# Kernel optimization log

Measured on AMD Instinct MI355X. Metric: run time of the kernel, lower is better.

Reference implementation:

```python
import jax, jax.numpy as jnp
import numpy as np

B, S, H2 = 32, 8192, 256  # batch, max_enc_steps, 2*hidden_dim
INIT_STD = 1e-4           # trunc_norm_init_std


def setup_inputs() -> dict:
    key = jax.random.key(0)
    k1, k2, k3 = jax.random.split(key, 3)
    h_d_t = jax.random.normal(k1, (B, H2), dtype=jnp.float32)
    h_enc = jax.random.normal(k2, (B, S, H2), dtype=jnp.float32)
    enc_padding_mask = jnp.ones((B, S), dtype=jnp.float32)
    sum_exp_att = jnp.ones((B, S), dtype=jnp.float32)
    # Bilinear weight (attn_dim=1 squeezed): (2H, 2H), trunc-normal init
    W = jax.random.normal(k3, (H2, H2), dtype=jnp.float32) * INIT_STD
    return {"h_d_t": h_d_t, "h_enc": h_enc, "enc_padding_mask": enc_padding_mask,
            "sum_exp_att": sum_exp_att, "W": W}


def reference(h_d_t, h_enc, enc_padding_mask, sum_exp_att, W):
    # Batched bilinear scores: score[b,s] = h_d_t[b] @ W @ h_enc[b,s]
    # replaces the per-timestep nn.Bilinear loop with one fused contraction.
    scores = jnp.einsum('bd,de,bse->bs', h_d_t, W, h_enc)  # (B, S)
    exp_att = jnp.exp(scores)
    # intra-temporal normalization by accumulated past exp attention
    att = exp_att / sum_exp_att
    new_sum_exp_att = sum_exp_att + exp_att
    # mask pads and renormalize
    alphat_e = att * enc_padding_mask
    alphat_e = alphat_e / jnp.sum(alphat_e, axis=1, keepdims=True)
    # context vector: weighted sum over encoder states
    ct_e = jnp.einsum('bs,bsd->bd', alphat_e, h_enc)  # (B, 2H)
    return ct_e, alphat_e, new_sum_exp_att
```

## Files before the change

### kernel.cpp

```cpp
#include <hip/hip_runtime.h>

#define B_ 32
#define S_ 8192
#define H_ 256

__global__ __launch_bounds__(256) void gemv_hdtW(
    const float* __restrict__ hdt,
    const float* __restrict__ W,
    float* __restrict__ v)
{
    const int b  = blockIdx.x;
    const int ec = blockIdx.y;
    const int d  = threadIdx.x;

    __shared__ float lh[32];
    if (d < 32) lh[d] = hdt[b * H_ + ec * 32 + d];
    __syncthreads();

    float acc = 0.f;
    const float* Wp = W + (size_t)(ec * 32) * H_ + d;
#pragma unroll
    for (int e = 0; e < 32; ++e) acc = fmaf(lh[e], Wp[(size_t)e * H_], acc);

    atomicAdd(&v[b * H_ + d], acc);
}

__global__ __launch_bounds__(256) void attn_main(
    const float* __restrict__ v,
    const float* __restrict__ h_enc,
    const float* __restrict__ sum_exp,
    const float* __restrict__ mask,
    float* __restrict__ out_alphat,
    float* __restrict__ out_newsum,
    float* __restrict__ denom,
    float* __restrict__ ct_un)
{
    constexpr int WAVES = 4;
    constexpr int SPB   = S_ / 32;

    const int b    = blockIdx.y;
    const int tid  = threadIdx.x;
    const int lane = tid & 63;
    const int wave = tid >> 6;
    const int s0   = blockIdx.x * SPB;

    const float4 vf = reinterpret_cast<const float4*>(v + b * H_)[lane];

    const float* __restrict__ hb  = h_enc  + (size_t)b * S_ * H_;
    const float* __restrict__ seb = sum_exp + (size_t)b * S_;
    const float* __restrict__ mkb = mask    + (size_t)b * S_;
    float* __restrict__ oab = out_alphat + (size_t)b * S_;
    float* __restrict__ onb = out_newsum + (size_t)b * S_;

    float4 ct  = {0.f, 0.f, 0.f, 0.f};
    float  den = 0.f;

    for (int i = 0; i < SPB / WAVES; ++i) {
        const int s = s0 + wave + WAVES * i;
        const float4 hf = reinterpret_cast<const float4*>(hb + (size_t)s * H_)[lane];

        float dot = fmaf(vf.x, hf.x, fmaf(vf.y, hf.y, fmaf(vf.z, hf.z, vf.w * hf.w)));
#pragma unroll
        for (int off = 32; off; off >>= 1) dot += __shfl_xor(dot, off, 64);

        const float se  = seb[s];
        const float e   = __expf(dot);
        const float att = e / se * mkb[s];

        if (lane == 0) {
            oab[s] = att;
            onb[s] = se + e;
        }
        den += att;
        ct.x = fmaf(att, hf.x, ct.x);
        ct.y = fmaf(att, hf.y, ct.y);
        ct.z = fmaf(att, hf.z, ct.z);
        ct.w = fmaf(att, hf.w, ct.w);
    }

    __shared__ __align__(16) float lct[WAVES * H_];
    __shared__ float lden[WAVES];
    reinterpret_cast<float4*>(lct + wave * H_)[lane] = ct;
    if (lane == 0) lden[wave] = den;
    __syncthreads();

    const float s4 = lct[tid] + lct[H_ + tid] + lct[2 * H_ + tid] + lct[3 * H_ + tid];
    atomicAdd(&ct_un[b * H_ + tid], s4);
    if (tid == 0) atomicAdd(&denom[b], lden[0] + lden[1] + lden[2] + lden[3]);
}

__global__ __launch_bounds__(256) void finalize(
    const float* __restrict__ denom,
    const float* __restrict__ ct_un,
    float* __restrict__ out_ct,
    float* __restrict__ out_alphat)
{
    const int idx = blockIdx.x * blockDim.x + threadIdx.x;
    if (idx < B_ * H_) {
        out_ct[idx] = ct_un[idx] / denom[idx >> 8];
    } else {
        const int p = idx - B_ * H_;
        if (p < B_ * S_) {
            out_alphat[p] = out_alphat[p] / denom[p >> 13];
        }
    }
}

extern "C" void kernel_launch(void* const* d_in, const int* in_sizes, int n_in,
                              void* d_out, int out_size, void* d_ws, size_t ws_size,
                              hipStream_t stream) {
    const float* h_d_t   = (const float*)d_in[0];
    const float* h_enc   = (const float*)d_in[1];
    const float* mask    = (const float*)d_in[2];
    const float* sum_exp = (const float*)d_in[3];
    const float* W       = (const float*)d_in[4];

    float* out        = (float*)d_out;
    float* out_ct     = out;
    float* out_alphat = out + B_ * H_;
    float* out_newsum = out + B_ * H_ + B_ * S_;

    float* ws    = (float*)d_ws;
    float* denom = ws;
    float* ct_un = ws + B_;
    float* v     = ws + B_ + B_ * H_;
    hipMemsetAsync(d_ws, 0, (size_t)(B_ + 2 * B_ * H_) * sizeof(float), stream);

    gemv_hdtW<<<dim3(B_, 8), 256, 0, stream>>>(h_d_t, W, v);
    attn_main<<<dim3(32, B_), 256, 0, stream>>>(v, h_enc, sum_exp, mask,
                                                out_alphat, out_newsum, denom, ct_un);
    const int fin_n = B_ * H_ + B_ * S_;
    finalize<<<(fin_n + 255) / 256, 256, 0, stream>>>(denom, ct_un, out_ct, out_alphat);
}
```

Baseline: 375.5 us.

## Split attention rows across 16-lane groups with smaller blocks and staged outputs

Restructures attn_main so that each 16-lane subgroup handles one encoder row, loading four float4s per lane. The dot-product reduction drops to four shuffles instead of six. Blocks now cover 128 rows rather than 256, which doubles the grid, and launch bounds request higher occupancy. The sum_exp and mask values are preloaded into shared memory, and alphat/newsum are staged there so they can be written back coalesced instead of by single lanes. The costs are more registers per thread, a 16-way shared-memory reduction of ct, and twice as many atomics.

```diff
diff --git a/kernel.cpp b/kernel.cpp
--- a/kernel.cpp
+++ b/kernel.cpp
@@ -3,6 +3,8 @@
 #define B_ 32
 #define S_ 8192
 #define H_ 256
+
+#define SPB 128
 
 __global__ __launch_bounds__(256) void gemv_hdtW(
     const float* __restrict__ hdt,
@@ -25,7 +27,7 @@
     atomicAdd(&v[b * H_ + d], acc);
 }
 
-__global__ __launch_bounds__(256) void attn_main(
+__global__ __launch_bounds__(256, 5) void attn_main(
     const float* __restrict__ v,
     const float* __restrict__ h_enc,
     const float* __restrict__ sum_exp,
@@ -35,58 +37,103 @@
     float* __restrict__ denom,
     float* __restrict__ ct_un)
 {
-    constexpr int WAVES = 4;
-    constexpr int SPB   = S_ / 32;
-
     const int b    = blockIdx.y;
     const int tid  = threadIdx.x;
     const int lane = tid & 63;
     const int wave = tid >> 6;
+    const int sub  = lane & 15;
+    const int grp  = lane >> 4;
+    const int pid  = wave * 4 + grp;
     const int s0   = blockIdx.x * SPB;
 
-    const float4 vf = reinterpret_cast<const float4*>(v + b * H_)[lane];
+    __shared__ float lmult[SPB];
+    __shared__ float lse[SPB];
+    __shared__ float lalpha[SPB];
+    __shared__ float lnew[SPB];
+    __shared__ __align__(16) float lct[16][H_];
+    __shared__ float lden[16];
 
-    const float* __restrict__ hb  = h_enc  + (size_t)b * S_ * H_;
-    const float* __restrict__ seb = sum_exp + (size_t)b * S_;
-    const float* __restrict__ mkb = mask    + (size_t)b * S_;
-    float* __restrict__ oab = out_alphat + (size_t)b * S_;
-    float* __restrict__ onb = out_newsum + (size_t)b * S_;
+    if (tid < SPB) {
+        const float se = sum_exp[(size_t)b * S_ + s0 + tid];
+        const float mk = mask[(size_t)b * S_ + s0 + tid];
+        lse[tid]   = se;
+        lmult[tid] = mk / se;
+    }
+    __syncthreads();
 
-    float4 ct  = {0.f, 0.f, 0.f, 0.f};
+    const float4* v4 = reinterpret_cast<const float4*>(v + b * H_);
+    const float4 vf0 = v4[0 * 16 + sub];
+    const float4 vf1 = v4[1 * 16 + sub];
+    const float4 vf2 = v4[2 * 16 + sub];
+    const float4 vf3 = v4[3 * 16 + sub];
+
+    const float* __restrict__ hb = h_enc + (size_t)b * S_ * H_;
+
+    float4 ct0 = {0.f,0.f,0.f,0.f}, ct1 = {0.f,0.f,0.f,0.f};
+    float4 ct2 = {0.f,0.f,0.f,0.f}, ct3 = {0.f,0.f,0.f,0.f};
     float  den = 0.f;
 
-    for (int i = 0; i < SPB / WAVES; ++i) {
-        const int s = s0 + wave + WAVES * i;
-        const float4 hf = reinterpret_cast<const float4*>(hb + (size_t)s * H_)[lane];
+#pragma unroll 2
+    for (int i = 0; i < SPB / 16; ++i) {
+        const int lr = i * 16 + wave * 4 + grp;
+        const float4* h4 = reinterpret_cast<const float4*>(hb + (size_t)(s0 + lr) * H_);
+        const float4 h0 = h4[0 * 16 + sub];
+        const float4 h1 = h4[1 * 16 + sub];
+        const float4 h2 = h4[2 * 16 + sub];
+        const float4 h3 = h4[3 * 16 + sub];
 
-        float dot = fmaf(vf.x, hf.x, fmaf(vf.y, hf.y, fmaf(vf.z, hf.z, vf.w * hf.w)));
-#pragma unroll
-        for (int off = 32; off; off >>= 1) dot += __shfl_xor(dot, off, 64);
+        float dot;
+        dot = fmaf(vf0.x, h0.x, fmaf(vf0.y, h0.y, fmaf(vf0.z, h0.z, vf0.w * h0.w)));
+        dot = fmaf(vf1.x, h1.x, fmaf(vf1.y, h1.y, fmaf(vf1.z, h1.z, fmaf(vf1.w, h1.w, dot))));
+        dot = fmaf(vf2.x, h2.x, fmaf(vf2.y, h2.y, fmaf(vf2.z, h2.z, fmaf(vf2.w, h2.w, dot))));
+        dot = fmaf(vf3.x, h3.x, fmaf(vf3.y, h3.y, fmaf(vf3.z, h3.z, fmaf(vf3.w, h3.w, dot))));
 
-        const float se  = seb[s];
+        dot += __shfl_xor(dot, 1, 16);
+        dot += __shfl_xor(dot, 2, 16);
+        dot += __shfl_xor(dot, 4, 16);
+        dot += __shfl_xor(dot, 8, 16);
+
         const float e   = __expf(dot);
-        const float att = e / se * mkb[s];
-
-        if (lane == 0) {
-            oab[s] = att;
-            onb[s] = se + e;
+        const float att = e * lmult[lr];
+        if (sub == 0) {
+            lalpha[lr] = att;
+            lnew[lr]   = lse[lr] + e;
         }
         den += att;
-        ct.x = fmaf(att, hf.x, ct.x);
-        ct.y = fmaf(att, hf.y, ct.y);
-        ct.z = fmaf(att, hf.z, ct.z);
-        ct.w = fmaf(att, hf.w, ct.w);
+        ct0.x = fmaf(att, h0.x, ct0.x); ct0.y = fmaf(att, h0.y, ct0.y);
+        ct0.z = fmaf(att, h0.z, ct0.z); ct0.w = fmaf(att, h0.w, ct0.w);
+        ct1.x = fmaf(att, h1.x, ct1.x); ct1.y = fmaf(att, h1.y, ct1.y);
+        ct1.z = fmaf(att, h1.z, ct1.z); ct1.w = fmaf(att, h1.w, ct1.w);
+        ct2.x = fmaf(att, h2.x, ct2.x); ct2.y = fmaf(att, h2.y, ct2.y);
+        ct2.z = fmaf(att, h2.z, ct2.z); ct2.w = fmaf(att, h2.w, ct2.w);
+        ct3.x = fmaf(att, h3.x, ct3.x); ct3.y = fmaf(att, h3.y, ct3.y);
+        ct3.z = fmaf(att, h3.z, ct3.z); ct3.w = fmaf(att, h3.w, ct3.w);
     }
 
-    __shared__ __align__(16) float lct[WAVES * H_];
-    __shared__ float lden[WAVES];
-    reinterpret_cast<float4*>(lct + wave * H_)[lane] = ct;
-    if (lane == 0) lden[wave] = den;
+    float4* dst = reinterpret_cast<float4*>(&lct[pid][0]);
+    dst[0 * 16 + sub] = ct0;
+    dst[1 * 16 + sub] = ct1;
+    dst[2 * 16 + sub] = ct2;
+    dst[3 * 16 + sub] = ct3;
+    if (sub == 0) lden[pid] = den;
     __syncthreads();
 
-    const float s4 = lct[tid] + lct[H_ + tid] + lct[2 * H_ + tid] + lct[3 * H_ + tid];
-    atomicAdd(&ct_un[b * H_ + tid], s4);
-    if (tid == 0) atomicAdd(&denom[b], lden[0] + lden[1] + lden[2] + lden[3]);
+    float tot = 0.f;
+#pragma unroll
+    for (int p = 0; p < 16; ++p) tot += lct[p][tid];
+    atomicAdd(&ct_un[b * H_ + tid], tot);
+
+    if (tid == 0) {
+        float d = 0.f;
+#pragma unroll
+        for (int p = 0; p < 16; ++p) d += lden[p];
+        atomicAdd(&denom[b], d);
+    }
+
+    if (tid < SPB) {
+        out_alphat[(size_t)b * S_ + s0 + tid] = lalpha[tid];
+        out_newsum[(size_t)b * S_ + s0 + tid] = lnew[tid];
+    }
 }
 
 __global__ __launch_bounds__(256) void finalize(
@@ -127,8 +174,8 @@
     hipMemsetAsync(d_ws, 0, (size_t)(B_ + 2 * B_ * H_) * sizeof(float), stream);
 
     gemv_hdtW<<<dim3(B_, 8), 256, 0, stream>>>(h_d_t, W, v);
-    attn_main<<<dim3(32, B_), 256, 0, stream>>>(v, h_enc, sum_exp, mask,
-                                                out_alphat, out_newsum, denom, ct_un);
+    attn_main<<<dim3(S_ / SPB, B_), 256, 0, stream>>>(v, h_enc, sum_exp, mask,
+                                                      out_alphat, out_newsum, denom, ct_un);
     const int fin_n = B_ * H_ + B_ * S_;
     finalize<<<(fin_n + 255) / 256, 256, 0, stream>>>(denom, ct_un, out_ct, out_alphat);
 }
```

Result: no change. 374.8 us (-0.2%).
